# Optimization experiments

Hardware: AMD Instinct MI355X
Metric: run time of the kernel (lower is better)

Reference implementation:

```python
import jax, jax.numpy as jnp
import numpy as np

L = 18                      # chain length -> Hilbert dim 2^L
J1 = 1.0                    # fixed exchange coupling (not trainable)
M_KRYLOV = 64               # Lanczos subspace size (>= n_eigs)
DIM = 2 ** L

# spin-1/2 operators (S = sigma/2)
SX = 0.5 * jnp.array([[0., 1.], [1., 0.]], jnp.float32)
SZ = 0.5 * jnp.array([[1., 0.], [0., -1.]], jnp.float32)
# two-site Heisenberg bond S_i.S_j in basis |00>,|01>,|10>,|11> (real: SxSx+SySy = flip terms)
BOND = jnp.array([[0.25, 0., 0., 0.],
                  [0., -0.25, 0.5, 0.],
                  [0., 0.5, -0.25, 0.],
                  [0., 0., 0., 0.25]], jnp.float32)


def setup_inputs() -> dict:
    key = jax.random.key(0)
    phi = jnp.asarray(2.0 * np.pi * np.arange(L) / L, jnp.float32)
    phi = phi + 0.01 * jax.random.normal(key, (L,), jnp.float32)
    return {
        "B_0": jnp.float32(0.2),
        "B_ext": jnp.float32(0.05),
        "phi_i": phi,
        "n_eigs": 4,
    }


def _matvec(v, field_ops):
    """Matrix-free H @ v for the open Heisenberg chain with site fields.
    v: (DIM,), field_ops: (L, 2, 2)."""
    out = jnp.zeros_like(v)
    bond = jnp.float32(J1) * BOND
    for i in range(L - 1):  # fixed structural loop over bonds
        blk = v.reshape(2 ** i, 4, 2 ** (L - i - 2))
        out = out + jnp.einsum('ab,xbz->xaz', bond, blk).reshape(-1)
    for i in range(L):      # fixed structural loop over sites (Zeeman term)
        blk = v.reshape(2 ** i, 2, 2 ** (L - i - 1))
        out = out + jnp.einsum('ab,xbz->xaz', field_ops[i], blk).reshape(-1)
    return out


def _lanczos(field_ops, v0, m):
    """m-step Lanczos; returns Krylov basis V (m, DIM) and tridiag coeffs."""
    def step(carry, _):
        v_prev, v, beta_prev = carry
        w = _matvec(v, field_ops)
        alpha = jnp.vdot(v, w)
        w = w - alpha * v - beta_prev * v_prev
        beta = jnp.sqrt(jnp.vdot(w, w))
        v_next = w / jnp.maximum(beta, jnp.float32(1e-12))
        return (v, v_next, beta), (v, alpha, beta)

    init = (jnp.zeros_like(v0), v0, jnp.float32(0.0))
    _, (V, alphas, betas) = jax.lax.scan(step, init, None, length=m)
    return V, alphas, betas


def reference(B_0, B_ext, phi_i, n_eigs):
    # skyrmion-texture field: in-plane/out-of-plane components from phi_i
    Bx = B_0 * jnp.sin(phi_i)
    Bz = B_0 * jnp.cos(phi_i) + B_ext
    field_ops = Bx[:, None, None] * SX + Bz[:, None, None] * SZ  # (L,2,2)

    v0 = jax.random.normal(jax.random.key(42), (DIM,), jnp.float32)  # v_init='randn'
    v0 = v0 / jnp.sqrt(jnp.vdot(v0, v0))

    V, a, b = _lanczos(field_ops, v0, M_KRYLOV)
    T = jnp.diag(a) + jnp.diag(b[:-1], 1) + jnp.diag(b[:-1], -1)  # (m,m) tridiag
    w, U = jnp.linalg.eigh(T)
    eigvals = w[:n_eigs]                                   # lowest n_eigs Ritz values
    eigvecs = jnp.einsum('md,mk->dk', V, U[:, :n_eigs])    # Ritz vectors (DIM, n_eigs)
    return eigvals, eigvecs
```

## Files before the change

### kernel.cpp

```cpp
#include <hip/hip_runtime.h>
#include <stdint.h>

#define L 18
#define DIM (1 << L)
#define MKRY 64
#define NBLK 256
#define TPB 1024

__device__ __forceinline__ uint32_t rotl32(uint32_t v, int r){ return (v<<r)|(v>>(32-r)); }

__device__ __forceinline__ void threefry2x32(uint32_t k0, uint32_t k1, uint32_t x0, uint32_t x1,
                                             uint32_t& o0, uint32_t& o1) {
  uint32_t k2 = k0 ^ k1 ^ 0x1BD11BDAu;
  x0 += k0; x1 += k1;
  x0+=x1; x1=rotl32(x1,13); x1^=x0;
  x0+=x1; x1=rotl32(x1,15); x1^=x0;
  x0+=x1; x1=rotl32(x1,26); x1^=x0;
  x0+=x1; x1=rotl32(x1,6);  x1^=x0;
  x0+=k1; x1+=k2+1u;
  x0+=x1; x1=rotl32(x1,17); x1^=x0;
  x0+=x1; x1=rotl32(x1,29); x1^=x0;
  x0+=x1; x1=rotl32(x1,16); x1^=x0;
  x0+=x1; x1=rotl32(x1,24); x1^=x0;
  x0+=k2; x1+=k0+2u;
  x0+=x1; x1=rotl32(x1,13); x1^=x0;
  x0+=x1; x1=rotl32(x1,15); x1^=x0;
  x0+=x1; x1=rotl32(x1,26); x1^=x0;
  x0+=x1; x1=rotl32(x1,6);  x1^=x0;
  x0+=k0; x1+=k1+3u;
  x0+=x1; x1=rotl32(x1,17); x1^=x0;
  x0+=x1; x1=rotl32(x1,29); x1^=x0;
  x0+=x1; x1=rotl32(x1,16); x1^=x0;
  x0+=x1; x1=rotl32(x1,24); x1^=x0;
  x0+=k1; x1+=k2+4u;
  x0+=x1; x1=rotl32(x1,13); x1^=x0;
  x0+=x1; x1=rotl32(x1,15); x1^=x0;
  x0+=x1; x1=rotl32(x1,26); x1^=x0;
  x0+=x1; x1=rotl32(x1,6);  x1^=x0;
  x0+=k2; x1+=k0+5u;
  o0=x0; o1=x1;
}

__device__ float jax_erfinv(float x){
  #pragma clang fp contract(off)
  float w = -log1pf(-x*x);
  float p;
  if (w < 5.0f) {
    w = w - 2.5f;
    p = 2.81022636e-08f;
    p = 3.43273939e-07f + p*w;
    p = -3.5233877e-06f + p*w;
    p = -4.39150654e-06f + p*w;
    p = 0.00021858087f + p*w;
    p = -0.00125372503f + p*w;
    p = -0.00417768164f + p*w;
    p = 0.246640727f + p*w;
    p = 1.50140941f + p*w;
  } else {
    w = sqrtf(w) - 3.0f;
    p = -0.000200214257f;
    p = 0.000100950558f + p*w;
    p = 0.00134934322f + p*w;
    p = -0.00367342844f + p*w;
    p = 0.00573950773f + p*w;
    p = -0.0076224613f + p*w;
    p = 0.00943887047f + p*w;
    p = 1.00167406f + p*w;
    p = 2.83297682f + p*w;
  }
  return p*x;
}

__device__ __forceinline__ float rng_val(unsigned i){
  #pragma clang fp contract(off)
  uint32_t o0,o1; threefry2x32(0u,42u,0u,i,o0,o1);
  uint32_t bits = o0 ^ o1;
  float f = __uint_as_float((bits >> 9) | 0x3f800000u) - 1.0f;
  const float lo = -0.99999994f;
  float u = f*2.0f;
  u = u + lo;
  u = fmaxf(lo, u);
  return 1.41421354f * jax_erfinv(u);
}

__device__ __forceinline__ double2 blockReduce2(double a, double b){
  __shared__ double sa[16], sb[16], res[2];
  int lane = threadIdx.x & 63, wid = threadIdx.x >> 6;
  #pragma unroll
  for (int off=32; off; off>>=1){ a += __shfl_down(a,off,64); b += __shfl_down(b,off,64); }
  if (lane==0){ sa[wid]=a; sb[wid]=b; }
  __syncthreads();
  if (wid==0){
    double xa = (lane<16)? sa[lane] : 0.0;
    double xb = (lane<16)? sb[lane] : 0.0;
    #pragma unroll
    for (int off=8; off; off>>=1){ xa += __shfl_down(xa,off,64); xb += __shfl_down(xb,off,64); }
    if (lane==0){ res[0]=xa; res[1]=xb; }
  }
  __syncthreads();
  double2 r; r.x=res[0]; r.y=res[1];
  return r;
}

__device__ __forceinline__ void p1_arrive(unsigned* bar){
  __hip_atomic_fetch_add(&bar[(blockIdx.x & 7)*32], 1u, __ATOMIC_ACQ_REL, __HIP_MEMORY_SCOPE_AGENT);
}
__device__ __forceinline__ void p1_wait_arrivals(unsigned* bar, unsigned target){
  unsigned guard=0;
  for (;;){
    unsigned sum=0;
    #pragma unroll
    for (int k=0;k<8;++k)
      sum += __hip_atomic_load(&bar[k*32], __ATOMIC_RELAXED, __HIP_MEMORY_SCOPE_AGENT);
    if (sum >= target) break;
    __builtin_amdgcn_s_sleep(1);
    if (++guard > (1u<<22)) break;
  }
  (void)__hip_atomic_load(&bar[0], __ATOMIC_ACQUIRE, __HIP_MEMORY_SCOPE_AGENT);
}
__device__ __forceinline__ void p1_spin(unsigned* ctr, unsigned target){
  unsigned guard=0;
  while (__hip_atomic_load(ctr, __ATOMIC_RELAXED, __HIP_MEMORY_SCOPE_AGENT) < target){
    __builtin_amdgcn_s_sleep(1);
    if (++guard > (1u<<22)) break;
  }
  (void)__hip_atomic_load(ctr, __ATOMIC_ACQUIRE, __HIP_MEMORY_SCOPE_AGENT);
}

__device__ __forceinline__ void gbar2(unsigned* bar, unsigned epoch){
  __syncthreads();
  if (threadIdx.x==0){
    const int st = (blockIdx.x & 7)*32;
    __hip_atomic_fetch_add(&bar[st], 1u, __ATOMIC_ACQ_REL, __HIP_MEMORY_SCOPE_AGENT);
    if (blockIdx.x==0){
      unsigned guard=0;
      for (;;){
        unsigned sum=0;
        #pragma unroll
        for (int k=0;k<8;++k)
          sum += __hip_atomic_load(&bar[k*32], __ATOMIC_ACQUIRE, __HIP_MEMORY_SCOPE_AGENT);
        if (sum >= (unsigned)NBLK) break;
        __builtin_amdgcn_s_sleep(1);
        if (++guard > (1u<<22)) break;
      }
      #pragma unroll
      for (int k=0;k<8;++k)
        __hip_atomic_store(&bar[k*32], 0u, __ATOMIC_RELAXED, __HIP_MEMORY_SCOPE_AGENT);
      __hip_atomic_fetch_add(&bar[256], 1u, __ATOMIC_RELEASE, __HIP_MEMORY_SCOPE_AGENT);
    } else {
      unsigned guard=0;
      while (__hip_atomic_load(&bar[256], __ATOMIC_RELAXED, __HIP_MEMORY_SCOPE_AGENT) < epoch){
        __builtin_amdgcn_s_sleep(1);
        if (++guard > (1u<<22)) break;
      }
      (void)__hip_atomic_load(&bar[256], __ATOMIC_ACQUIRE, __HIP_MEMORY_SCOPE_AGENT);
    }
  }
  __syncthreads();
}

#define CM_INIT {3u<<16,3u<<15,3u<<14,3u<<13,3u<<12,3u<<11,3u<<10,3u<<9, \
                 1u<<17,1u<<16,1u<<15,1u<<14,1u<<13,1u<<12,1u<<11,1u<<10}

__device__ __forceinline__ float matvec1(int s, int tid, float vs,
                                         const float* __restrict__ lds_v,
                                         const float (*__restrict__ lds_hv)[TPB],
                                         const float* __restrict__ hxz){
  #pragma clang fp contract(off)
  float acc = 0.0f;
  #pragma unroll
  for (int i=0;i<L-1;++i){
    const int q = L-2-i;
    const unsigned msk = 3u<<q;
    const unsigned b2 = ((unsigned)s >> q) & 3u;
    float nbv;
    if (i<=7) nbv = lds_hv[i][tid];
    else      nbv = lds_v[((unsigned)s ^ msk) & (TPB-1u)];
    if (b2==0u || b2==3u){ acc = acc + 0.25f*vs; }
    else if (b2==1u){ float t = -0.25f*vs; t = t + 0.5f*nbv; acc = acc + t; }
    else            { float t = 0.5f*nbv; t = t + (-0.25f)*vs; acc = acc + t; }
  }
  #pragma unroll
  for (int i=0;i<L;++i){
    const int p = L-1-i;
    const unsigned msk = 1u<<p;
    const float hx = hxz[i], hz = hxz[18+i];
    float nbv;
    if (i<=7) nbv = lds_hv[8+i][tid];
    else      nbv = lds_v[((unsigned)s ^ msk) & (TPB-1u)];
    float t;
    if ((unsigned)s & msk){ t = hx*nbv; t = t + (-hz)*vs; }
    else                  { t = hz*vs;  t = t + hx*nbv; }
    acc = acc + t;
  }
  return acc;
}


__global__ void k_init(unsigned* bar){ int t=threadIdx.x; if (t<1024) bar[t]=0u; }

__global__ void __launch_bounds__(TPB) k_pass1(const float* __restrict__ B0,
        const float* __restrict__ Bext, const float* __restrict__ phi,
        float* __restrict__ vbase, int vmod, float* __restrict__ wring,
        double* __restrict__ part, float* scal, unsigned* bar){
  __shared__ float lds_v[TPB];
  __shared__ float lds_hv[16][TPB];
  __shared__ float lds_hvp[16][TPB];
  __shared__ float lds_hxz[36];
  const unsigned CM[16] = CM_INIT;
  const int tid = threadIdx.x, bid = blockIdx.x;
  const int s = bid*TPB + tid;

  if (bid==0 && tid < L){
    #pragma clang fp contract(off)
    float b0 = B0[0], be = Bext[0];
    double ph = (double)phi[tid];
    float Bx = b0*(float)sin(ph);
    float Bz = b0*(float)cos(ph);
    Bz = Bz + be;
    scal[130+tid] = 0.5f*Bx;
    scal[148+tid] = 0.5f*Bz;
  }

  float n = rng_val((unsigned)s);
  {
    double2 pr = blockReduce2((double)n*(double)n, 0.0);
    if (tid==0){ part[512+2*bid]=pr.x; part[512+2*bid+1]=pr.y; }
  }
  float nrm;
  if (bid==0){
    if (tid==0){
      p1_arrive(bar);
      p1_wait_arrivals(bar, (unsigned)NBLK*1u);
      __hip_atomic_fetch_add(&bar[288], 1u, __ATOMIC_RELEASE, __HIP_MEMORY_SCOPE_AGENT);
    }
    __syncthreads();
    double xa = (tid<NBLK)? part[512+2*tid] : 0.0;
    double xb = (tid<NBLK)? part[512+2*tid+1] : 0.0;
    double2 t2 = blockReduce2(xa, xb);
    nrm = (float)sqrt(t2.x);
    if (tid==0){
      scal[129] = nrm;
      __hip_atomic_fetch_add(&bar[256], 1u, __ATOMIC_RELEASE, __HIP_MEMORY_SCOPE_AGENT);
    }
  } else {
    if (tid==0){
      p1_arrive(bar);
      p1_spin(&bar[256], 1u);
    }
    __syncthreads();
    nrm = scal[129];
  }

  if (tid < 36) lds_hxz[tid] = scal[130+tid];

  float v = __fdiv_rn(n, nrm), vp = 0.0f, b_p = 0.0f;
  vbase[s] = v;

  #pragma unroll
  for (int ci=0; ci<16; ++ci){
    lds_hv[ci][tid]  = __fdiv_rn(rng_val((unsigned)s ^ CM[ci]), nrm);
    lds_hvp[ci][tid] = 0.0f;
  }
  lds_v[tid] = v;
  __syncthreads();

  for (int m=0; m<MKRY; ++m){
    float w = matvec1(s, tid, v, lds_v, lds_hv, lds_hxz);
    wring[(size_t)(m&1)*DIM + s] = w;

    double2 p2 = blockReduce2((double)v*(double)w, (double)w*(double)w);
    double* pb = part + (size_t)(m&1)*512;
    if (tid==0){ pb[2*bid]=p2.x; pb[2*bid+1]=p2.y; }

    const unsigned e = 2u + (unsigned)m;
    const float* wr = wring + (size_t)(m&1)*DIM;
    float wn[16];
    float alpha, beta;

    if (bid==0){
      if (tid==0){
        p1_arrive(bar);
        p1_wait_arrivals(bar, (unsigned)NBLK*e);
        __hip_atomic_fetch_add(&bar[288], 1u, __ATOMIC_RELEASE, __HIP_MEMORY_SCOPE_AGENT);
      }
      __syncthreads();
      double xa = (tid<NBLK)? pb[2*tid] : 0.0;
      double xb = (tid<NBLK)? pb[2*tid+1] : 0.0;
      double2 tt = blockReduce2(xa, xb);
      alpha = (float)tt.x;
      double b2d = tt.y - tt.x*tt.x - (double)b_p*(double)b_p;
      beta = (float)sqrt(fmax(b2d, 0.0));
      if (tid==0){
        scal[m] = alpha; scal[64+m] = beta;
        __hip_atomic_fetch_add(&bar[256], 1u, __ATOMIC_RELEASE, __HIP_MEMORY_SCOPE_AGENT);
      }
      #pragma unroll
      for (int ci=0; ci<16; ++ci) wn[ci] = wr[(unsigned)s ^ CM[ci]];
    } else {
      if (tid==0){
        p1_arrive(bar);
        p1_spin(&bar[288], e);
      }
      __syncthreads();
      #pragma unroll
      for (int ci=0; ci<16; ++ci) wn[ci] = wr[(unsigned)s ^ CM[ci]];
      if (tid==0){
        p1_spin(&bar[256], e);
      }
      __syncthreads();
      alpha = scal[m]; beta = scal[64+m];
    }
    float bden = fmaxf(beta, 1e-12f);

    float vn;
    {
      #pragma clang fp contract(off)
      float x = w - alpha*v;
      x = x - b_p*vp;
      vn = __fdiv_rn(x, bden);
    }
    vbase[(size_t)((m+1)%vmod)*DIM + s] = vn;

    #pragma unroll
    for (int ci=0; ci<16; ++ci){
      #pragma clang fp contract(off)
      float hv = lds_hv[ci][tid];
      float x = wn[ci] - alpha*hv;
      x = x - b_p*lds_hvp[ci][tid];
      float hn = __fdiv_rn(x, bden);
      lds_hvp[ci][tid] = hv;
      lds_hv[ci][tid] = hn;
    }

    vp=v; v=vn; b_p=beta;
    lds_v[tid]=vn;
    __syncthreads();
  }
}

__global__ void __launch_bounds__(256) k_pass2s(const float* __restrict__ vbase,
        const float* __restrict__ scal, float* __restrict__ out){
  __shared__ float U[256];
  int tid = threadIdx.x;
  int s = blockIdx.x*256 + tid;
  U[tid] = scal[192+tid];
  __syncthreads();
  {
    #pragma clang fp contract(off)
    float o0=0.0f,o1=0.0f,o2=0.0f,o3=0.0f;
    for (int m=0;m<MKRY;++m){
      float vm = vbase[(size_t)m*DIM + s];
      o0 = o0 + vm*U[4*m+0];
      o1 = o1 + vm*U[4*m+1];
      o2 = o2 + vm*U[4*m+2];
      o3 = o3 + vm*U[4*m+3];
    }
    *(float4*)(out + 4 + 4*(size_t)s) = make_float4(o0,o1,o2,o3);
  }
}

__global__ void __launch_bounds__(TPB) k_pass2c(float* __restrict__ wring,
        const float* __restrict__ scal, float* __restrict__ out, unsigned* barc){
  __shared__ float lds_v[TPB];
  __shared__ float lds_hv[16][TPB];
  __shared__ float lds_hvp[16][TPB];
  __shared__ float lds_hxz[36];
  __shared__ float lds_ab[384];
  const unsigned CM[16] = CM_INIT;
  const int tid = threadIdx.x, bid = blockIdx.x;
  const int s = bid*TPB + tid;
  if (tid < 36) lds_hxz[tid] = scal[130+tid];
  if (tid < 128) lds_ab[tid] = scal[tid];
  if (tid >= 128 && tid < 384) lds_ab[tid] = scal[192 + (tid-128)];
  const float nrm = scal[129];
  float v = __fdiv_rn(rng_val((unsigned)s), nrm), vp = 0.0f;
  #pragma unroll
  for (int ci=0; ci<16; ++ci){
    lds_hv[ci][tid]  = __fdiv_rn(rng_val((unsigned)s ^ CM[ci]), nrm);
    lds_hvp[ci][tid] = 0.0f;
  }
  lds_v[tid] = v;
  __syncthreads();
  float o0=0.0f,o1=0.0f,o2=0.0f,o3=0.0f;
  for (int m=0;m<MKRY;++m){
    float w = matvec1(s, tid, v, lds_v, lds_hv, lds_hxz);
    wring[(size_t)(m&1)*DIM + s] = w;
    {
      #pragma clang fp contract(off)
      o0 = o0 + v*lds_ab[128+4*m+0];
      o1 = o1 + v*lds_ab[128+4*m+1];
      o2 = o2 + v*lds_ab[128+4*m+2];
      o3 = o3 + v*lds_ab[128+4*m+3];
    }
    gbar2(barc, 1+(unsigned)m);
    float wn[16];
    const float* wr = wring + (size_t)(m&1)*DIM;
    #pragma unroll
    for (int ci=0; ci<16; ++ci) wn[ci] = wr[(unsigned)s ^ CM[ci]];
    float alpha = lds_ab[m];
    float bp = (m==0)? 0.0f : lds_ab[64+m-1];
    float bden = fmaxf(lds_ab[64+m], 1e-12f);
    float vn;
    {
      #pragma clang fp contract(off)
      float x = w - alpha*v;
      x = x - bp*vp;
      vn = __fdiv_rn(x, bden);
    }
    #pragma unroll
    for (int ci=0; ci<16; ++ci){
      #pragma clang fp contract(off)
      float hv = lds_hv[ci][tid];
      float x = wn[ci] - alpha*hv;
      x = x - bp*lds_hvp[ci][tid];
      float hn = __fdiv_rn(x, bden);
      lds_hvp[ci][tid] = hv;
      lds_hv[ci][tid] = hn;
    }
    vp=v; v=vn;
    lds_v[tid]=vn;
    __syncthreads();
  }
  *(float4*)(out + 4 + 4*(size_t)s) = make_float4(o0,o1,o2,o3);
}

__global__ void k_eigh(float* __restrict__ scal, float* __restrict__ out){
  __shared__ double Z[64][65];
  int t = threadIdx.x;
  double ddv = (double)scal[t];
  double eev = (t<63)? (double)scal[64+t] : 0.0;
  for (int j=0;j<64;++j) Z[t][j] = (t==j)?1.0:0.0;
  __syncthreads();

  for (int l=0;l<64;++l){
    for (int iter=0; iter<80; ++iter){
      double dt1 = __shfl_down(ddv, 1, 64);
      bool cond = (t>=l) && (t<63) &&
                  (fabs(eev) <= 2.220446049250313e-16 * (fabs(ddv)+fabs(dt1)));
      unsigned long long bm = __ballot(cond) | (1ull<<63);
      int m = (int)__builtin_ctzll(bm);
      if (m==l) break;
      double dd_l  = __shfl(ddv, l, 64);
      double dd_l1 = __shfl(ddv, l+1, 64);
      double dd_m  = __shfl(ddv, m, 64);
      double ee_l  = __shfl(eev, l, 64);
      double g = (dd_l1-dd_l)/(2.0*ee_l);
      double r = sqrt(fma(g,g,1.0));
      g = dd_m-dd_l + ee_l/(g + copysign(r,g));
      double s=1.0, c=1.0, p=0.0;
      int stop = l;
      double ee_i  = __shfl(eev, m-1, 64);
      double dd_i  = __shfl(ddv, m-1, 64);
      double dd_i1 = dd_m;
      double zhi = Z[t][m];
      for (int i=m-1; i>=l; --i){
        double ee_n=0.0, dd_n=0.0;
        if (i>l){ ee_n = __shfl(eev, i-1, 64); dd_n = __shfl(ddv, i-1, 64); }
        double f = s*ee_i, b = c*ee_i;
        double h = fma(f,f,g*g);
        if (h==0.0){
          if (t==i+1) ddv = dd_i1 - p;
          if (t==m) eev = 0.0;
          stop = i+1;
          break;
        }
        double inv;
        if (h < 1e-35){
          inv = 1.0/sqrt(h);
        } else {
          double x0 = (double)__frsqrt_rn((float)h);
          inv = x0*(1.5 - (0.5*h)*(x0*x0));
        }
        s = f*inv; c = g*inv;
        double rr = h*inv;
        g = dd_i1 - p;
        double r2 = (dd_i - g)*s + 2.0*c*b;
        p = s*r2;
        double ddw = g + p;
        g = c*r2 - b;
        if (t==i+1){ ddv = ddw; eev = rr; }
        double zlo = Z[t][i];
        Z[t][i+1] = s*zlo + c*zhi;
        zhi = c*zlo - s*zhi;
        dd_i1 = dd_i; ee_i = ee_n; dd_i = dd_n;
        if (i==l){
          if (t==l){ ddv = ddv - p; eev = g; }
          if (t==m){ eev = 0.0; }
        }
      }
      Z[t][stop] = zhi;
      __syncthreads();
    }
  }
  double dvm = ddv;
  #pragma unroll
  for (int k=0;k<4;++k){
    double mv = dvm; int mi = t;
    #pragma unroll
    for (int off=32; off; off>>=1){
      double ov = __shfl_down(mv, off, 64);
      int    oi = __shfl_down(mi, off, 64);
      if (ov < mv || (ov==mv && oi<mi)){ mv=ov; mi=oi; }
    }
    int jm = __shfl(mi, 0, 64);
    double lv = __shfl(mv, 0, 64);
    if (t==jm) dvm = 1.0e300;
    scal[192 + t*4 + k] = (float)Z[t][jm];
    if (t==k) out[k] = (float)lv;
  }
}

extern "C" void kernel_launch(void* const* d_in, const int* in_sizes, int n_in,
                              void* d_out, int out_size, void* d_ws, size_t ws_size,
                              hipStream_t stream){
  (void)in_sizes; (void)n_in; (void)out_size;
  const float* B0   = (const float*)d_in[0];
  const float* Bext = (const float*)d_in[1];
  const float* phi  = (const float*)d_in[2];
  float* out = (float*)d_out;

  size_t need_big = ((size_t)(MKRY+3)*DIM)*4 + 16384;
  int vmod; bool big;
  if (ws_size >= need_big) { vmod = MKRY+1; big = true; }
  else                     { vmod = 3;      big = false; }

  float* vbase = (float*)d_ws;
  float* wring = vbase + (size_t)vmod*DIM;
  double* part = (double*)(wring + 2*(size_t)DIM);
  float* scal  = (float*)(part + 1024);
  unsigned* bar = (unsigned*)(scal + 512);

  hipLaunchKernelGGL(k_init, dim3(1), dim3(1024), 0, stream, bar);
  {
    void* args[] = { (void*)&B0, (void*)&Bext, (void*)&phi,
                     (void*)&vbase, (void*)&vmod, (void*)&wring,
                     (void*)&part, (void*)&scal, (void*)&bar };
    (void)hipLaunchCooperativeKernel((const void*)k_pass1, dim3(NBLK), dim3(TPB), args, 0, stream);
  }
  hipLaunchKernelGGL(k_eigh, dim3(1), dim3(64), 0, stream, scal, out);
  if (big){
    hipLaunchKernelGGL(k_pass2s, dim3(DIM/256), dim3(256), 0, stream, vbase, scal, out);
  } else {
    unsigned* barc = bar + 512;
    void* args[] = { (void*)&wring, (void*)&scal, (void*)&out, (void*)&barc };
    (void)hipLaunchCooperativeKernel((const void*)k_pass2c, dim3(NBLK), dim3(TPB), args, 0, stream);
  }
}
```

Before: 2.368 ms.

## Split tridiagonal QL eigensolver into rotation and eigenvector-update wavefronts

The single-wave implicit QL eigensolver for the 64x64 tridiagonal matrix is split across two wavefronts. Wave 0 computes the Givens rotations for each QL sweep and stores them in double-buffered shared memory. Wave 1 applies the previous sweep's rotations to the eigenvector matrix Z, so the two run in a software pipeline. The goal is to take the Z updates, with their LDS reads and writes, off the serial critical path of the rotation recurrence, at the cost of a block-wide barrier every step and extra shared-memory traffic.

```diff
diff --git a/kernel.cpp b/kernel.cpp
--- a/kernel.cpp
+++ b/kernel.cpp
@@ -425,89 +425,124 @@
   *(float4*)(out + 4 + 4*(size_t)s) = make_float4(o0,o1,o2,o3);
 }
 
-__global__ void k_eigh(float* __restrict__ scal, float* __restrict__ out){
+__global__ void __launch_bounds__(128) k_eigh(float* __restrict__ scal, float* __restrict__ out){
   __shared__ double Z[64][65];
-  int t = threadIdx.x;
-  double ddv = (double)scal[t];
-  double eev = (t<63)? (double)scal[64+t] : 0.0;
-  for (int j=0;j<64;++j) Z[t][j] = (t==j)?1.0:0.0;
-  __syncthreads();
-
-  for (int l=0;l<64;++l){
-    for (int iter=0; iter<80; ++iter){
-      double dt1 = __shfl_down(ddv, 1, 64);
-      bool cond = (t>=l) && (t<63) &&
-                  (fabs(eev) <= 2.220446049250313e-16 * (fabs(ddv)+fabs(dt1)));
-      unsigned long long bm = __ballot(cond) | (1ull<<63);
-      int m = (int)__builtin_ctzll(bm);
-      if (m==l) break;
-      double dd_l  = __shfl(ddv, l, 64);
-      double dd_l1 = __shfl(ddv, l+1, 64);
-      double dd_m  = __shfl(ddv, m, 64);
-      double ee_l  = __shfl(eev, l, 64);
-      double g = (dd_l1-dd_l)/(2.0*ee_l);
-      double r = sqrt(fma(g,g,1.0));
-      g = dd_m-dd_l + ee_l/(g + copysign(r,g));
-      double s=1.0, c=1.0, p=0.0;
-      int stop = l;
-      double ee_i  = __shfl(eev, m-1, 64);
-      double dd_i  = __shfl(ddv, m-1, 64);
-      double dd_i1 = dd_m;
-      double zhi = Z[t][m];
-      for (int i=m-1; i>=l; --i){
-        double ee_n=0.0, dd_n=0.0;
-        if (i>l){ ee_n = __shfl(eev, i-1, 64); dd_n = __shfl(ddv, i-1, 64); }
-        double f = s*ee_i, b = c*ee_i;
-        double h = fma(f,f,g*g);
-        if (h==0.0){
-          if (t==i+1) ddv = dd_i1 - p;
-          if (t==m) eev = 0.0;
-          stop = i+1;
-          break;
+  __shared__ double ssb[2][64], ccb[2][64];
+  __shared__ int meta_m[2], meta_stop[2];
+  const int t = threadIdx.x;
+  const int r = t & 63;
+  const bool w0 = (t < 64);
+
+  double ddv = 0.0, eev = 0.0;
+  if (w0){
+    ddv = (double)scal[r];
+    eev = (r<63)? (double)scal[64+r] : 0.0;
+    for (int j=0;j<64;++j) Z[r][j] = (r==j)?1.0:0.0;
+  }
+  __syncthreads();
+
+  int l = 0;
+  for (int step=0; step<12000; ++step){
+    const int pb = step & 1;
+    const int cb = pb ^ 1;
+    if (w0){
+      int m_out = -1, stop_out = 0;
+      while (l < 64){
+        double dt1 = __shfl_down(ddv, 1, 64);
+        bool cond = (r>=l) && (r<63) &&
+                    (fabs(eev) <= 2.220446049250313e-16 * (fabs(ddv)+fabs(dt1)));
+        unsigned long long bm = __ballot(cond) | (1ull<<63);
+        int m = (int)__builtin_ctzll(bm);
+        if (m==l){ ++l; continue; }
+        double dd_l  = __shfl(ddv, l, 64);
+        double dd_l1 = __shfl(ddv, l+1, 64);
+        double dd_m  = __shfl(ddv, m, 64);
+        double ee_l  = __shfl(eev, l, 64);
+        double g = (dd_l1-dd_l)/(2.0*ee_l);
+        double r0 = sqrt(fma(g,g,1.0));
+        g = dd_m-dd_l + ee_l/(g + copysign(r0,g));
+        double s=1.0, c=1.0, p=0.0;
+        int stop = l;
+        double ee_i  = __shfl(eev, m-1, 64);
+        double dd_i  = __shfl(ddv, m-1, 64);
+        double dd_i1 = dd_m;
+        for (int i=m-1; i>=l; --i){
+          double ee_n=0.0, dd_n=0.0;
+          if (i>l){ ee_n = __shfl(eev, i-1, 64); dd_n = __shfl(ddv, i-1, 64); }
+          double f = s*ee_i, b = c*ee_i;
+          double h = fma(f,f,g*g);
+          if (h==0.0){
+            if (r==i+1) ddv = dd_i1 - p;
+            if (r==m) eev = 0.0;
+            stop = i+1;
+            break;
+          }
+          double inv;
+          if (h < 1e-35){
+            inv = 1.0/sqrt(h);
+          } else {
+            double x0 = (double)__frsqrt_rn((float)h);
+            inv = x0*(1.5 - (0.5*h)*(x0*x0));
+          }
+          s = f*inv; c = g*inv;
+          double rr = h*inv;
+          g = dd_i1 - p;
+          double r2 = (dd_i - g)*s + 2.0*c*b;
+          p = s*r2;
+          double ddw = g + p;
+          g = c*r2 - b;
+          if (r==i+1){ ddv = ddw; eev = rr; }
+          if (r==i){ ssb[pb][r] = s; ccb[pb][r] = c; }
+          dd_i1 = dd_i; ee_i = ee_n; dd_i = dd_n;
+          if (i==l){
+            if (r==l){ ddv = ddv - p; eev = g; }
+            if (r==m){ eev = 0.0; }
+          }
         }
-        double inv;
-        if (h < 1e-35){
-          inv = 1.0/sqrt(h);
-        } else {
-          double x0 = (double)__frsqrt_rn((float)h);
-          inv = x0*(1.5 - (0.5*h)*(x0*x0));
+        m_out = m; stop_out = stop;
+        break;
+      }
+      if (r==0){ meta_m[pb] = m_out; meta_stop[pb] = stop_out; }
+    } else {
+      if (step > 0){
+        int m = meta_m[cb], stop = meta_stop[cb];
+        if (m >= 0){
+          double zhi = Z[r][m];
+          if (m-1 >= stop){
+            double sI = ssb[cb][m-1], cI = ccb[cb][m-1], zlo = Z[r][m-1];
+            for (int i=m-1; i>=stop; --i){
+              double sN=0.0, cN=0.0, zN=0.0;
+              if (i>stop){ sN=ssb[cb][i-1]; cN=ccb[cb][i-1]; zN=Z[r][i-1]; }
+              Z[r][i+1] = sI*zlo + cI*zhi;
+              zhi = cI*zlo - sI*zhi;
+              sI=sN; cI=cN; zlo=zN;
+            }
+          }
+          Z[r][stop] = zhi;
         }
-        s = f*inv; c = g*inv;
-        double rr = h*inv;
-        g = dd_i1 - p;
-        double r2 = (dd_i - g)*s + 2.0*c*b;
-        p = s*r2;
-        double ddw = g + p;
-        g = c*r2 - b;
-        if (t==i+1){ ddv = ddw; eev = rr; }
-        double zlo = Z[t][i];
-        Z[t][i+1] = s*zlo + c*zhi;
-        zhi = c*zlo - s*zhi;
-        dd_i1 = dd_i; ee_i = ee_n; dd_i = dd_n;
-        if (i==l){
-          if (t==l){ ddv = ddv - p; eev = g; }
-          if (t==m){ eev = 0.0; }
-        }
-      }
-      Z[t][stop] = zhi;
-      __syncthreads();
-    }
-  }
-  double dvm = ddv;
-  #pragma unroll
-  for (int k=0;k<4;++k){
-    double mv = dvm; int mi = t;
+      }
+    }
+    __syncthreads();
+    if (meta_m[pb] == -1) break;
+  }
+
+  if (w0){
+    double dvm = ddv;
     #pragma unroll
-    for (int off=32; off; off>>=1){
-      double ov = __shfl_down(mv, off, 64);
-      int    oi = __shfl_down(mi, off, 64);
-      if (ov < mv || (ov==mv && oi<mi)){ mv=ov; mi=oi; }
-    }
-    int jm = __shfl(mi, 0, 64);
-    double lv = __shfl(mv, 0, 64);
-    if (t==jm) dvm = 1.0e300;
-    scal[192 + t*4 + k] = (float)Z[t][jm];
-    if (t==k) out[k] = (float)lv;
+    for (int k=0;k<4;++k){
+      double mv = dvm; int mi = r;
+      #pragma unroll
+      for (int off=32; off; off>>=1){
+        double ov = __shfl_down(mv, off, 64);
+        int    oi = __shfl_down(mi, off, 64);
+        if (ov < mv || (ov==mv && oi<mi)){ mv=ov; mi=oi; }
+      }
+      int jm = __shfl(mi, 0, 64);
+      double lv = __shfl(mv, 0, 64);
+      if (r==jm) dvm = 1.0e300;
+      scal[192 + r*4 + k] = (float)Z[r][jm];
+      if (r==k) out[k] = (float)lv;
+    }
   }
 }
 
@@ -538,7 +573,7 @@
                      (void*)&part, (void*)&scal, (void*)&bar };
     (void)hipLaunchCooperativeKernel((const void*)k_pass1, dim3(NBLK), dim3(TPB), args, 0, stream);
   }
-  hipLaunchKernelGGL(k_eigh, dim3(1), dim3(64), 0, stream, scal, out);
+  hipLaunchKernelGGL(k_eigh, dim3(1), dim3(128), 0, stream, scal, out);
   if (big){
     hipLaunchKernelGGL(k_pass2s, dim3(DIM/256), dim3(256), 0, stream, vbase, scal, out);
   } else {
```

Result: slower. 2.610 ms (+10.2%).
